# Optimization experiments

Hardware: AMD Instinct MI355X
Metric: run time of the kernel (lower is better)

Reference implementation:

```python
import jax, jax.numpy as jnp
import numpy as np

IMAGE_SIZE = 224          # config.image_size
RP_Q = 10 / 100.0         # config.rp_percentage, 'point' threshold mode
EPS = 1e-8                # normalize_minmax eps
CLIP = 1e-6               # arccos clamp margin


def minmax_global(x):
    """normalize_minmax over the whole tensor (as applied to the raw series)."""
    lo, hi = x.min(), x.max()
    rng = hi - lo
    return jnp.where(rng < EPS, jnp.zeros_like(x), (x - lo) / (rng + EPS))


def minmax_per_matrix(x):
    """normalize_minmax applied independently per (b, d) LxL matrix."""
    lo = x.min(axis=(-2, -1), keepdims=True)
    hi = x.max(axis=(-2, -1), keepdims=True)
    rng = hi - lo
    return jnp.where(rng < EPS, jnp.zeros_like(x), (x - lo) / (rng + EPS))


def setup_inputs() -> dict:
    key = jax.random.key(0)
    x = jax.random.normal(key, (4, 1024, 8), dtype=jnp.float32)  # [B, L, D]
    return {"x": x}


def reference(x):
    B, L, D = x.shape

    # ---- Gramian Angular Field (summation), vectorized over (b, d) ----
    x_norm = minmax_global(x) * 2.0 - 1.0                       # [B, L, D]
    theta = jnp.arccos(jnp.clip(x_norm, -1.0 + CLIP, 1.0 - CLIP))
    th = jnp.transpose(theta, (0, 2, 1))                        # [B, D, L]
    gaf = jnp.cos(th[:, :, :, None] + th[:, :, None, :])        # [B, D, L, L]
    gaf = minmax_per_matrix(gaf)

    # ---- Recurrence plot ('point' quantile threshold), vectorized ----
    s = jnp.transpose(x, (0, 2, 1))                             # [B, D, L]
    dist = jnp.abs(s[:, :, :, None] - s[:, :, None, :])         # [B, D, L, L]
    thr = jnp.quantile(dist.reshape(B, D, L * L), RP_Q, axis=-1)
    rp = (dist <= thr[:, :, None, None]).astype(x.dtype)        # [B, D, L, L]

    # ---- Bilinear resize to (image_size, image_size), align_corners=False ----
    out = jnp.concatenate([gaf, rp], axis=1)                    # [B, 2D, L, L]
    out = jax.image.resize(out, (B, 2 * D, IMAGE_SIZE, IMAGE_SIZE),
                           method="bilinear", antialias=False)
    return out
```

## Files before the change

kernel.cpp:

```cpp
#include <hip/hip_runtime.h>
#include <cfloat>
#include <math.h>

#define B_ 4
#define L_ 1024
#define D_ 8
#define OUT_ 224
#define NPIX (B_ * 2 * D_ * OUT_ * OUT_)
#define NT4  (NPIX / 4)
#define PI_F 3.14159265358979323846f
#define TBL 128
#define TSTR 896

__device__ __forceinline__ float clipnorm(float v, float lo, float inv2, int degen) {
    float xn = degen ? -1.0f : ((v - lo) * inv2 - 1.0f);
    return fminf(fmaxf(xn, -1.0f + 1e-6f), 1.0f - 1e-6f);
}
__device__ __forceinline__ unsigned fkey(float f) {
    unsigned u = __float_as_uint(f);
    return (u & 0x80000000u) ? ~u : (u | 0x80000000u);
}
__device__ __forceinline__ float unfkey(unsigned k) {
    unsigned u = (k & 0x80000000u) ? (k ^ 0x80000000u) : ~k;
    return __uint_as_float(u);
}

__global__ __launch_bounds__(1024) void k_stats(const float* __restrict__ x,
                                                float* __restrict__ ws) {
    __shared__ float t[L_];
    __shared__ float csort[L_], ssort[L_], w[L_];
    __shared__ unsigned part[2][16];
    __shared__ unsigned umin_a, umax_a, umin_b, umax_b, succ_bits;
    __shared__ unsigned cand_n;
    __shared__ float cand[64];
    __shared__ float bc_v1v2[2];

    const int tid  = threadIdx.x;
    const int lane = tid & 63;
    const int wave = tid >> 6;
    const int blk  = blockIdx.x;
    const int b = blk >> 3, d = blk & 7;

    if (tid == 0) {
        umin_a = 0xFFFFFFFFu; umax_a = 0u;
        umin_b = 0xFFFFFFFFu; umax_b = 0u;
        succ_bits = 0xFFFFFFFFu;
        cand_n = 0u;
    }
    __syncthreads();

    {
        const float4* x4 = (const float4*)x;
        float lo = FLT_MAX, hi = -FLT_MAX;
        for (int i = tid; i < (B_ * L_ * D_) / 4; i += 1024) {
            float4 q = x4[i];
            lo = fminf(fminf(fminf(lo, q.x), q.y), fminf(q.z, q.w));
            hi = fmaxf(fmaxf(fmaxf(hi, q.x), q.y), fmaxf(q.z, q.w));
        }
#pragma unroll
        for (int off = 32; off; off >>= 1) {
            lo = fminf(lo, __shfl_down(lo, off));
            hi = fmaxf(hi, __shfl_down(hi, off));
        }
        if (lane == 0) { atomicMin(&umin_a, fkey(lo)); atomicMax(&umax_a, fkey(hi)); }
    }
    __syncthreads();
    const float glo = unfkey(umin_a), ghi = unfkey(umax_a);
    if (blk == 0 && tid == 0) { ws[0] = glo; ws[1] = ghi; }
    const float rng  = ghi - glo;
    const int degen  = rng < 1e-8f;
    const float inv2 = 2.0f / (rng + 1e-8f);

    if (tid < 2 * OUT_) {
        const float scale = (float)L_ / (float)OUT_;
        int o = (tid < OUT_) ? tid : tid - OUT_;
        float fx = (o + 0.5f) * scale - 0.5f;
        int x0 = (int)fx; float wx = fx - (float)x0;
        float q0 = x[(b * L_ + x0) * D_ + d];
        float q1 = x[(b * L_ + x0 + 1) * D_ + d];
        float* base = ws + TBL + blk * TSTR;
        if (tid < OUT_) {
            float c0 = clipnorm(q0, glo, inv2, degen), c1 = clipnorm(q1, glo, inv2, degen);
            float s0 = sqrtf(fmaxf(0.0f, 1.0f - c0 * c0)), s1 = sqrtf(fmaxf(0.0f, 1.0f - c1 * c1));
            base[o]        = c0 + wx * (c1 - c0);
            base[OUT_ + o] = s0 + wx * (s1 - s0);
        } else {
            base[448 + o] = q0;
            base[672 + o] = q1;
        }
    }

    float v = x[(b * L_ + tid) * D_ + d];
    for (int k = 2; k <= L_; k <<= 1) {
        bool up = ((tid & k) == 0);
        for (int j = k >> 1; j > 0; j >>= 1) {
            bool lower = ((tid & j) == 0);
            float other;
            if (j >= 64) {
                __syncthreads();
                t[tid] = v;
                __syncthreads();
                other = t[tid ^ j];
            } else {
                other = __shfl_xor(v, j);
            }
            float mn = fminf(v, other), mx = fmaxf(v, other);
            v = (lower == up) ? mn : mx;
        }
    }
    __syncthreads();
    t[tid] = v;
    {
        float c = clipnorm(v, glo, inv2, degen);
        csort[tid] = c;
        ssort[tid] = sqrtf(fmaxf(0.0f, 1.0f - c * c));
        w[tid]     = acosf(c);
    }
    __syncthreads();

    {
        float wi = w[tid];
        int jstar = -1;
        if (wi + w[0] >= PI_F) {
            int a = 0, bh = L_ - 1;
            while (a < bh) { int m = (a + bh + 1) >> 1; if (wi + w[m] >= PI_F) a = m; else bh = m - 1; }
            jstar = a;
        }
        float ci = csort[tid], si = ssort[tid];
        float mn = FLT_MAX, mx = -FLT_MAX;
        int cands[4] = {0, L_ - 1, jstar, jstar + 1};
#pragma unroll
        for (int q = 0; q < 4; q++) {
            int j = cands[q];
            if (j >= 0 && j < L_) {
                float g = ci * csort[j] - si * ssort[j];
                mn = fminf(mn, g); mx = fmaxf(mx, g);
            }
        }
#pragma unroll
        for (int off = 32; off; off >>= 1) {
            mn = fminf(mn, __shfl_down(mn, off));
            mx = fmaxf(mx, __shfl_down(mx, off));
        }
        if (lane == 0) { atomicMin(&umin_b, fkey(mn)); atomicMax(&umax_b, fkey(mx)); }
        __syncthreads();
        if (tid == 0) {
            ws[2 + blk * 3 + 0] = unfkey(umin_b);
            ws[2 + blk * 3 + 1] = unfkey(umax_b);
        }
    }

    const float ti = v;
    int pass = 0;
    auto block_count = [&](unsigned c) -> unsigned {
#pragma unroll
        for (int off = 32; off; off >>= 1) c += __shfl_down(c, off);
        int pb = pass & 1;
        if (lane == 0) part[pb][wave] = c;
        __syncthreads();
        unsigned tot = 0;
#pragma unroll
        for (int w2 = 0; w2 < 16; w2++) tot += part[pb][w2];
        pass++;
        return tot;
    };

    int jloA_, jhiA_;
    {
        int aL = 0, bL = tid, aH = tid, bH = L_ - 1;
        while ((aL < bL) | (aH < bH)) {
            int mL = (aL + bL) >> 1;
            int mH = (aH + bH + 1) >> 1;
            float tL = t[aL < bL ? mL : 0];
            float tH = t[aH < bH ? mH : 0];
            if (aL < bL) { if (ti - tL <= 0.0f) bL = mL; else aL = mL + 1; }
            if (aH < bH) { if (tH - ti <= 0.0f) aH = mH; else bH = mH - 1; }
        }
        jloA_ = aL; jhiA_ = aH;
    }

    const unsigned k1 = 104858u, k2 = 104859u;
    unsigned c0 = block_count((unsigned)(jhiA_ - jloA_ + 1));

    float thr;
    if (c0 >= k1) {
        if (c0 >= k2) thr = 0.0f;
        else {
            float s = FLT_MAX;
            if (jloA_ > 0)      s = fminf(s, ti - t[jloA_ - 1]);
            if (jhiA_ < L_ - 1) s = fminf(s, t[jhiA_ + 1] - ti);
#pragma unroll
            for (int off = 32; off; off >>= 1) s = fminf(s, __shfl_down(s, off));
            if (lane == 0) atomicMin(&succ_bits, __float_as_uint(s));
            __syncthreads();
            thr = 0.5f * __uint_as_float(succ_bits);
        }
    } else {
        unsigned aBits = 0u, bBits = __float_as_uint(t[L_ - 1] - t[0]);
        unsigned cntLo = c0, cntHi = (unsigned)(L_ * L_);
        int jloB_ = 0, jhiB_ = L_ - 1;
        float sga = (float)((long long)c0 - (long long)k1);
        float sgb = (float)((long long)(L_ * L_) - (long long)k1);
        int lastSide = 0, sameCnt = 0;

        while ((bBits - aBits > 1u) && (cntHi - cntLo > 63u)) {
            unsigned mb;
            if (sameCnt >= 3) {
                mb = aBits + ((bBits - aBits) >> 1);
                sameCnt = 0;
            } else {
                float va = __uint_as_float(aBits), vb = __uint_as_float(bBits);
                float vg = va - sga * (vb - va) / (sgb - sga);
                mb = __float_as_uint(vg);
                if (mb <= aBits) mb = aBits + 1u;
                else if (mb >= bBits) mb = bBits - 1u;
            }
            float vm = __uint_as_float(mb);
            int aL = jloB_, bL = jloA_, aH = jhiA_, bH = jhiB_;
            while ((aL < bL) | (aH < bH)) {
                int mL = (aL + bL) >> 1;
                int mH = (aH + bH + 1) >> 1;
                float tL = t[aL < bL ? mL : 0];
                float tH = t[aH < bH ? mH : 0];
                if (aL < bL) { if (ti - tL <= vm) bL = mL; else aL = mL + 1; }
                if (aH < bH) { if (tH - ti <= vm) aH = mH; else bH = mH - 1; }
            }
            unsigned tot = block_count((unsigned)(aH - aL + 1));
            long long g = (long long)tot - (long long)k1;
            if (g >= 0) {
                bBits = mb; cntHi = tot; jloB_ = aL; jhiB_ = aH;
                sgb = fmaxf((float)g, 0.5f);
                if (lastSide == 1) { sga *= 0.5f; sameCnt++; } else sameCnt = 1;
                lastSide = 1;
            } else {
                aBits = mb; cntLo = tot; jloA_ = aL; jhiA_ = aH;
                sga = fminf((float)g, -0.5f);
                if (lastSide == -1) { sgb *= 0.5f; sameCnt++; } else sameCnt = 1;
                lastSide = -1;
            }
        }

        if (cntHi - cntLo <= 63u) {
            for (int j = jloB_; j < jloA_; j++) { unsigned p = atomicAdd(&cand_n, 1u); cand[p] = ti - t[j]; }
            for (int j = jhiA_ + 1; j <= jhiB_; j++) { unsigned p = atomicAdd(&cand_n, 1u); cand[p] = t[j] - ti; }
            __syncthreads();
            if (tid < 64) {
                unsigned n = cand_n;
                float val = ((unsigned)tid < n) ? cand[tid] : FLT_MAX;
#pragma unroll
                for (int k = 2; k <= 64; k <<= 1) {
                    bool up = ((tid & k) == 0);
#pragma unroll
                    for (int j = k >> 1; j > 0; j >>= 1) {
                        float o = __shfl_xor(val, j);
                        bool lower = ((tid & j) == 0);
                        float mn = fminf(val, o), mx = fmaxf(val, o);
                        val = (lower == up) ? mn : mx;
                    }
                }
                unsigned r1 = k1 - cntLo, r2 = k2 - cntLo;
                float v1l = __shfl(val, (int)r1 - 1);
                float v2l = (r2 <= n) ? __shfl(val, (int)r2 - 1) : FLT_MAX;
                if (tid == 0) { bc_v1v2[0] = v1l; bc_v1v2[1] = v2l; }
            }
            __syncthreads();
            float v1 = bc_v1v2[0], v2m = bc_v1v2[1];
            if (v2m < FLT_MAX) {
                thr = v1 + (v2m - v1) * 0.5f;
            } else {
                float s = FLT_MAX;
                if (jloB_ > 0)      s = fminf(s, ti - t[jloB_ - 1]);
                if (jhiB_ < L_ - 1) s = fminf(s, t[jhiB_ + 1] - ti);
#pragma unroll
                for (int off = 32; off; off >>= 1) s = fminf(s, __shfl_down(s, off));
                if (lane == 0) atomicMin(&succ_bits, __float_as_uint(s));
                __syncthreads();
                float v2 = __uint_as_float(succ_bits);
                thr = v1 + (v2 - v1) * 0.5f;
            }
        } else {
            float v1 = __uint_as_float(bBits);
            if (cntHi >= k2) {
                thr = v1;
            } else {
                float s = FLT_MAX;
                if (jloB_ > 0)      s = fminf(s, ti - t[jloB_ - 1]);
                if (jhiB_ < L_ - 1) s = fminf(s, t[jhiB_ + 1] - ti);
#pragma unroll
                for (int off = 32; off; off >>= 1) s = fminf(s, __shfl_down(s, off));
                if (lane == 0) atomicMin(&succ_bits, __float_as_uint(s));
                __syncthreads();
                float v2 = __uint_as_float(succ_bits);
                thr = v1 + (v2 - v1) * 0.5f;
            }
        }
    }
    if (tid == 0) ws[2 + blk * 3 + 2] = thr;
}

__global__ __launch_bounds__(256) void k_out(const float* __restrict__ ws,
                                             float4* __restrict__ out4) {
    __shared__ __align__(16) float lds[448];
    __shared__ float sc[3];

    const int tid = threadIdx.x;
    int plane = blockIdx.x / 49;
    int c = plane & 15, b = plane >> 4, d = c & 7;

    const float* tb = ws + TBL + (b * 8 + d) * TSTR + ((c < 8) ? 0 : 448);
    for (int i = tid; i < 448; i += 256) lds[i] = tb[i];
    if (tid == 0) {
        if (c < 8) {
            float mn = ws[2 + (b * 8 + d) * 3 + 0];
            float mx = ws[2 + (b * 8 + d) * 3 + 1];
            float g = mx - mn;
            sc[0] = mn;
            sc[1] = (g < 1e-8f) ? 0.0f : 1.0f / (g + 1e-8f);
            sc[2] = (g < 1e-8f) ? 1.0f : 0.0f;
        } else {
            sc[0] = ws[2 + (b * 8 + d) * 3 + 2];
        }
    }
    __syncthreads();

    int tix = blockIdx.x * 256 + tid;
    int pix0 = tix << 2;
    int ox0 = pix0 % OUT_;
    int oy  = (pix0 / OUT_) % OUT_;

    float4 r;
    if (c < 8) {
        float mn = sc[0], ginv = sc[1];
        bool gdeg = sc[2] != 0.0f;
        float Cr = lds[oy], Sr = lds[OUT_ + oy];
        float4 Cc = *(const float4*)&lds[ox0];
        float4 Sc = *(const float4*)&lds[OUT_ + ox0];
        r.x = gdeg ? 0.0f : ((Cr * Cc.x - Sr * Sc.x) - mn) * ginv;
        r.y = gdeg ? 0.0f : ((Cr * Cc.y - Sr * Sc.y) - mn) * ginv;
        r.z = gdeg ? 0.0f : ((Cr * Cc.z - Sr * Sc.z) - mn) * ginv;
        r.w = gdeg ? 0.0f : ((Cr * Cc.w - Sr * Sc.w) - mn) * ginv;
    } else {
        float thr = sc[0];
        const float scale = (float)L_ / (float)OUT_;
        float fy = (oy + 0.5f) * scale - 0.5f;
        int y0 = (int)fy; float wy = fy - (float)y0;
        float r0 = lds[oy], r1 = lds[OUT_ + oy];
        float4 q0 = *(const float4*)&lds[ox0];
        float4 q1 = *(const float4*)&lds[OUT_ + ox0];
        float qq0[4] = {q0.x, q0.y, q0.z, q0.w};
        float qq1[4] = {q1.x, q1.y, q1.z, q1.w};
        float res[4];
#pragma unroll
        for (int p = 0; p < 4; p++) {
            float fx = (ox0 + p + 0.5f) * scale - 0.5f;
            int x0i = (int)fx; float wx = fx - (float)x0i;
            float v00 = (fabsf(r0 - qq0[p]) <= thr) ? 1.0f : 0.0f;
            float v01 = (fabsf(r0 - qq1[p]) <= thr) ? 1.0f : 0.0f;
            float v10 = (fabsf(r1 - qq0[p]) <= thr) ? 1.0f : 0.0f;
            float v11 = (fabsf(r1 - qq1[p]) <= thr) ? 1.0f : 0.0f;
            float top = v00 + wx * (v01 - v00);
            float bot = v10 + wx * (v11 - v10);
            res[p] = top + wy * (bot - top);
        }
        r = make_float4(res[0], res[1], res[2], res[3]);
    }
    out4[tix] = r;
}

extern "C" void kernel_launch(void* const* d_in, const int* in_sizes, int n_in,
                              void* d_out, int out_size, void* d_ws, size_t ws_size,
                              hipStream_t stream) {
    const float* x = (const float*)d_in[0];
    float* ws = (float*)d_ws;

    k_stats<<<B_ * D_, 1024, 0, stream>>>(x, ws);
    k_out<<<NT4 / 256, 256, 0, stream>>>(ws, (float4*)d_out);
}
```

Before: 96.94 us.

## Replace per-plane sort/bisection quantile with histogram-based multi-kernel selection

Swaps the single 32-block stats kernel (bitonic sort plus iterative count bisection) for a three-kernel pipeline. The first kernel spreads the O(L^2) pairwise distances across 512 blocks to build distance histograms and GAF min/max. The second collects candidates falling in the bins around the target rank, and the third refines by sub-histogram to select the quantile. It uses the output buffer as scratch before k_out overwrites it. This aims to raise parallelism over the serialized bisection, at the cost of brute-force pair work, LDS atomics, extra launches, and a fixed candidate cap (CAP) that could overflow.

```diff
diff --git a/kernel.cpp b/kernel.cpp
--- a/kernel.cpp
+++ b/kernel.cpp
@@ -8,294 +8,402 @@
 #define OUT_ 224
 #define NPIX (B_ * 2 * D_ * OUT_ * OUT_)
 #define NT4  (NPIX / 4)
-#define PI_F 3.14159265358979323846f
 #define TBL 128
 #define TSTR 896
+
+#define NPLANE 32
+#define PB 16
+#define NBLK (NPLANE * PB)
+#define NBIN 2048
+#define CAP 8192
+#define R1U 51917u
+#define R2U 51918u
+
+#define SC_PHIST 0u
+#define SC_PGAF  ((unsigned)NBLK * (unsigned)NBIN)
+#define SC_CCNT  (SC_PGAF + (unsigned)NBLK * 2u)
+#define SC_BBC   (SC_CCNT + (unsigned)NPLANE)
+#define SC_CAND  (SC_BBC + (unsigned)NPLANE * 4u)
 
 __device__ __forceinline__ float clipnorm(float v, float lo, float inv2, int degen) {
     float xn = degen ? -1.0f : ((v - lo) * inv2 - 1.0f);
     return fminf(fmaxf(xn, -1.0f + 1e-6f), 1.0f - 1e-6f);
 }
-__device__ __forceinline__ unsigned fkey(float f) {
-    unsigned u = __float_as_uint(f);
-    return (u & 0x80000000u) ? ~u : (u | 0x80000000u);
-}
-__device__ __forceinline__ float unfkey(unsigned k) {
-    unsigned u = (k & 0x80000000u) ? (k ^ 0x80000000u) : ~k;
-    return __uint_as_float(u);
-}
-
-__global__ __launch_bounds__(1024) void k_stats(const float* __restrict__ x,
-                                                float* __restrict__ ws) {
-    __shared__ float t[L_];
-    __shared__ float csort[L_], ssort[L_], w[L_];
-    __shared__ unsigned part[2][16];
-    __shared__ unsigned umin_a, umax_a, umin_b, umax_b, succ_bits;
-    __shared__ unsigned cand_n;
-    __shared__ float cand[64];
-    __shared__ float bc_v1v2[2];
+
+__device__ __forceinline__ float sort64(float val, int tid) {
+#pragma unroll
+    for (int k = 2; k <= 64; k <<= 1) {
+        bool up = ((tid & k) == 0);
+#pragma unroll
+        for (int j = k >> 1; j > 0; j >>= 1) {
+            float o = __shfl_xor(val, j);
+            bool lower = ((tid & j) == 0);
+            float mn = fminf(val, o), mx = fmaxf(val, o);
+            val = (lower == up) ? mn : mx;
+        }
+    }
+    return val;
+}
+
+__global__ __launch_bounds__(256) void k_pairs(const float* __restrict__ x,
+                                               float* __restrict__ ws,
+                                               unsigned* __restrict__ scratch) {
+    __shared__ float s[L_], cc[L_], ssn[L_];
+    __shared__ unsigned hist[NBIN];
+    __shared__ float red[16];
 
     const int tid  = threadIdx.x;
     const int lane = tid & 63;
     const int wave = tid >> 6;
-    const int blk  = blockIdx.x;
-    const int b = blk >> 3, d = blk & 7;
-
+    const int bid  = blockIdx.x;
+    const int p    = bid >> 4;
+    const int bip  = bid & 15;
+    const int b    = p >> 3, d = p & 7;
+
+    float lo = FLT_MAX, hi = -FLT_MAX;
+    const float4* x4 = (const float4*)x;
+    for (int i = tid; i < (B_ * L_ * D_) / 4; i += 256) {
+        float4 q = x4[i];
+        lo = fminf(fminf(fminf(lo, q.x), q.y), fminf(q.z, q.w));
+        hi = fmaxf(fmaxf(fmaxf(hi, q.x), q.y), fmaxf(q.z, q.w));
+    }
+#pragma unroll
+    for (int off = 32; off; off >>= 1) {
+        lo = fminf(lo, __shfl_down(lo, off));
+        hi = fmaxf(hi, __shfl_down(hi, off));
+    }
+    if (lane == 0) { red[wave] = lo; red[8 + wave] = hi; }
+    __syncthreads();
+    const float glo = fminf(fminf(red[0], red[1]), fminf(red[2], red[3]));
+    const float ghi = fmaxf(fmaxf(red[8], red[9]), fmaxf(red[10], red[11]));
+    const float rng   = ghi - glo;
+    const int   degen = rng < 1e-8f;
+    const float inv2  = 2.0f / (rng + 1e-8f);
+    const float scale = (float)(NBIN - 1) / fmaxf(rng, 1e-20f);
+
+    if (bid == 0) {
+        if (tid == 0) { ws[0] = glo; ws[1] = ghi; }
+        if (tid < NPLANE) scratch[SC_CCNT + tid] = 0u;
+    }
+
+    for (int i = tid; i < L_; i += 256) {
+        float v = x[(b * L_ + i) * D_ + d];
+        float c = clipnorm(v, glo, inv2, degen);
+        s[i] = v; cc[i] = c; ssn[i] = sqrtf(fmaxf(0.0f, 1.0f - c * c));
+    }
+    for (int i = tid; i < NBIN; i += 256) hist[i] = 0u;
+    __syncthreads();
+
+    float sj[4], cj[4], zj[4];
+#pragma unroll
+    for (int q = 0; q < 4; q++) {
+        int j = tid + q * 256;
+        sj[q] = s[j]; cj[q] = cc[j]; zj[q] = ssn[j];
+    }
+    float gmn = FLT_MAX, gmx = -FLT_MAX;
+#pragma unroll
+    for (int q = 0; q < 4; q++) {
+        float g = cj[q] * cj[q] - zj[q] * zj[q];
+        gmn = fminf(gmn, g); gmx = fmaxf(gmx, g);
+    }
+
+    for (int rp = 0; rp < 64; ++rp) {
+        int i = (rp < 32) ? (bip * 32 + rp) : (L_ - 1 - (bip * 32 + rp - 32));
+        float siv = s[i], civ = cc[i], ziv = ssn[i];
+#pragma unroll
+        for (int q = 0; q < 4; q++) {
+            int j = tid + q * 256;
+            if (j > i) {
+                float dd = fabsf(siv - sj[q]);
+                int bin = (int)(dd * scale);
+                bin = min(bin, NBIN - 1);
+                atomicAdd(&hist[bin], 1u);
+                float g = civ * cj[q] - ziv * zj[q];
+                gmn = fminf(gmn, g); gmx = fmaxf(gmx, g);
+            }
+        }
+    }
+    __syncthreads();
+
+    {
+        unsigned* ph = scratch + SC_PHIST + (unsigned)bid * NBIN;
+        for (int i = tid; i < NBIN; i += 256) ph[i] = hist[i];
+    }
+#pragma unroll
+    for (int off = 32; off; off >>= 1) {
+        gmn = fminf(gmn, __shfl_down(gmn, off));
+        gmx = fmaxf(gmx, __shfl_down(gmx, off));
+    }
+    if (lane == 0) { red[wave] = gmn; red[8 + wave] = gmx; }
+    __syncthreads();
     if (tid == 0) {
-        umin_a = 0xFFFFFFFFu; umax_a = 0u;
-        umin_b = 0xFFFFFFFFu; umax_b = 0u;
-        succ_bits = 0xFFFFFFFFu;
-        cand_n = 0u;
-    }
-    __syncthreads();
-
-    {
-        const float4* x4 = (const float4*)x;
-        float lo = FLT_MAX, hi = -FLT_MAX;
-        for (int i = tid; i < (B_ * L_ * D_) / 4; i += 1024) {
-            float4 q = x4[i];
-            lo = fminf(fminf(fminf(lo, q.x), q.y), fminf(q.z, q.w));
-            hi = fmaxf(fmaxf(fmaxf(hi, q.x), q.y), fmaxf(q.z, q.w));
-        }
-#pragma unroll
-        for (int off = 32; off; off >>= 1) {
-            lo = fminf(lo, __shfl_down(lo, off));
-            hi = fmaxf(hi, __shfl_down(hi, off));
-        }
-        if (lane == 0) { atomicMin(&umin_a, fkey(lo)); atomicMax(&umax_a, fkey(hi)); }
-    }
-    __syncthreads();
-    const float glo = unfkey(umin_a), ghi = unfkey(umax_a);
-    if (blk == 0 && tid == 0) { ws[0] = glo; ws[1] = ghi; }
-    const float rng  = ghi - glo;
-    const int degen  = rng < 1e-8f;
-    const float inv2 = 2.0f / (rng + 1e-8f);
-
-    if (tid < 2 * OUT_) {
-        const float scale = (float)L_ / (float)OUT_;
-        int o = (tid < OUT_) ? tid : tid - OUT_;
-        float fx = (o + 0.5f) * scale - 0.5f;
-        int x0 = (int)fx; float wx = fx - (float)x0;
-        float q0 = x[(b * L_ + x0) * D_ + d];
-        float q1 = x[(b * L_ + x0 + 1) * D_ + d];
-        float* base = ws + TBL + blk * TSTR;
-        if (tid < OUT_) {
+        float* pg = (float*)scratch + SC_PGAF + bid * 2;
+        pg[0] = fminf(fminf(red[0], red[1]), fminf(red[2], red[3]));
+        pg[1] = fmaxf(fmaxf(red[8], red[9]), fmaxf(red[10], red[11]));
+    }
+
+    if (bip == 0) {
+        const float scL = (float)L_ / (float)OUT_;
+        float* base = ws + TBL + p * TSTR;
+        for (int o = tid; o < OUT_; o += 256) {
+            float fx = (o + 0.5f) * scL - 0.5f;
+            int x0 = (int)fx; float wx = fx - (float)x0;
+            float q0 = x[(b * L_ + x0) * D_ + d];
+            float q1 = x[(b * L_ + x0 + 1) * D_ + d];
             float c0 = clipnorm(q0, glo, inv2, degen), c1 = clipnorm(q1, glo, inv2, degen);
             float s0 = sqrtf(fmaxf(0.0f, 1.0f - c0 * c0)), s1 = sqrtf(fmaxf(0.0f, 1.0f - c1 * c1));
             base[o]        = c0 + wx * (c1 - c0);
             base[OUT_ + o] = s0 + wx * (s1 - s0);
-        } else {
-            base[448 + o] = q0;
-            base[672 + o] = q1;
-        }
-    }
-
-    float v = x[(b * L_ + tid) * D_ + d];
-    for (int k = 2; k <= L_; k <<= 1) {
-        bool up = ((tid & k) == 0);
-        for (int j = k >> 1; j > 0; j >>= 1) {
-            bool lower = ((tid & j) == 0);
-            float other;
-            if (j >= 64) {
-                __syncthreads();
-                t[tid] = v;
-                __syncthreads();
-                other = t[tid ^ j];
-            } else {
-                other = __shfl_xor(v, j);
-            }
-            float mn = fminf(v, other), mx = fmaxf(v, other);
-            v = (lower == up) ? mn : mx;
-        }
-    }
-    __syncthreads();
-    t[tid] = v;
-    {
-        float c = clipnorm(v, glo, inv2, degen);
-        csort[tid] = c;
-        ssort[tid] = sqrtf(fmaxf(0.0f, 1.0f - c * c));
-        w[tid]     = acosf(c);
-    }
-    __syncthreads();
-
-    {
-        float wi = w[tid];
-        int jstar = -1;
-        if (wi + w[0] >= PI_F) {
-            int a = 0, bh = L_ - 1;
-            while (a < bh) { int m = (a + bh + 1) >> 1; if (wi + w[m] >= PI_F) a = m; else bh = m - 1; }
-            jstar = a;
-        }
-        float ci = csort[tid], si = ssort[tid];
-        float mn = FLT_MAX, mx = -FLT_MAX;
-        int cands[4] = {0, L_ - 1, jstar, jstar + 1};
+            base[448 + o]  = q0;
+            base[672 + o]  = q1;
+        }
+    }
+}
+
+__global__ __launch_bounds__(256) void k_collect(const float* __restrict__ x,
+                                                 const float* __restrict__ ws,
+                                                 unsigned* __restrict__ scratch) {
+    __shared__ float s[L_];
+    __shared__ unsigned cwsum[4];
+    __shared__ unsigned sB1, sB2, sBase;
+
+    const int tid  = threadIdx.x;
+    const int lane = tid & 63;
+    const int wave = tid >> 6;
+    const int bid  = blockIdx.x;
+    const int p    = bid >> 4;
+    const int bip  = bid & 15;
+    const int b    = p >> 3, d = p & 7;
+
+    const float glo = ws[0], ghi = ws[1];
+    const float scale = (float)(NBIN - 1) / fmaxf(ghi - glo, 1e-20f);
+
+    for (int i = tid; i < L_; i += 256) s[i] = x[(b * L_ + i) * D_ + d];
+
+    unsigned loc[8];
+#pragma unroll
+    for (int q = 0; q < 8; q++) loc[q] = 0u;
+    const unsigned* ph = scratch + SC_PHIST + (unsigned)(p * PB) * NBIN;
+    for (int k = 0; k < PB; k++) {
+        const unsigned* hh = ph + k * NBIN + tid * 8;
+#pragma unroll
+        for (int q = 0; q < 8; q++) loc[q] += hh[q];
+    }
+    unsigned tsum = 0u;
+#pragma unroll
+    for (int q = 0; q < 8; q++) tsum += loc[q];
+    unsigned inc = tsum;
+#pragma unroll
+    for (int off = 1; off < 64; off <<= 1) {
+        unsigned o = __shfl_up(inc, off);
+        if (lane >= off) inc += o;
+    }
+    if (lane == 63) cwsum[wave] = inc;
+    __syncthreads();
+    unsigned woff = 0u;
+    for (int w2 = 0; w2 < 4; w2++) woff += (w2 < wave) ? cwsum[w2] : 0u;
+    unsigned run = woff + inc - tsum;
+#pragma unroll
+    for (int q = 0; q < 8; q++) {
+        unsigned prev = run; run += loc[q];
+        if (prev < R1U && run >= R1U) { sB1 = (unsigned)(tid * 8 + q); sBase = prev; }
+        if (prev < R2U && run >= R2U) { sB2 = (unsigned)(tid * 8 + q); }
+    }
+    __syncthreads();
+    const unsigned B1 = sB1, B2 = sB2;
+    if (bip == 0 && tid == 0) {
+        unsigned* bbc = scratch + SC_BBC + (unsigned)p * 4u;
+        bbc[0] = B1; bbc[1] = B2; bbc[2] = sBase;
+    }
+
+    float sj[4];
+#pragma unroll
+    for (int q = 0; q < 4; q++) sj[q] = s[tid + q * 256];
+
+    unsigned* ccnt = scratch + SC_CCNT + p;
+    float* cand = (float*)scratch + SC_CAND + (unsigned)p * CAP;
+    for (int rp = 0; rp < 64; ++rp) {
+        int i = (rp < 32) ? (bip * 32 + rp) : (L_ - 1 - (bip * 32 + rp - 32));
+        float siv = s[i];
 #pragma unroll
         for (int q = 0; q < 4; q++) {
-            int j = cands[q];
-            if (j >= 0 && j < L_) {
-                float g = ci * csort[j] - si * ssort[j];
-                mn = fminf(mn, g); mx = fmaxf(mx, g);
-            }
-        }
-#pragma unroll
-        for (int off = 32; off; off >>= 1) {
+            int j = tid + q * 256;
+            if (j > i) {
+                float dd = fabsf(siv - sj[q]);
+                int bin = (int)(dd * scale);
+                bin = min(bin, NBIN - 1);
+                if (bin >= (int)B1 && bin <= (int)B2) {
+                    unsigned idx = atomicAdd(ccnt, 1u);
+                    if (idx < CAP) cand[idx] = dd;
+                }
+            }
+        }
+    }
+}
+
+__global__ __launch_bounds__(1024) void k_select(float* __restrict__ ws,
+                                                 unsigned* __restrict__ scratch) {
+    __shared__ float cd[CAP];
+    __shared__ float buf2[2048];
+    __shared__ unsigned h[1024];
+    __shared__ unsigned wsum[16], wsum2[16];
+    __shared__ unsigned sT1, sT2, sC1, sH1, scnt, uminb, umaxb;
+    __shared__ float sv1, sv2;
+
+    const int tid  = threadIdx.x;
+    const int lane = tid & 63;
+    const int wave = tid >> 6;
+    const int p    = blockIdx.x;
+
+    const float glo = ws[0], ghi = ws[1];
+    const float scale = (float)(NBIN - 1) / fmaxf(ghi - glo, 1e-20f);
+    const unsigned* bbc = scratch + SC_BBC + (unsigned)p * 4u;
+    const unsigned B1 = bbc[0], B2 = bbc[1], base = bbc[2];
+    unsigned n = scratch[SC_CCNT + p];
+    n = (n < (unsigned)CAP) ? n : (unsigned)CAP;
+    const float* cand = (const float*)scratch + SC_CAND + (unsigned)p * CAP;
+    for (unsigned k = tid; k < n; k += 1024) cd[k] = cand[k];
+
+    float* cur = cd;
+    float* nxt = buf2;
+    unsigned ncur = n;
+    unsigned r1 = R1U - base;
+    float vlo = (float)B1 / scale;
+    float vhi = (float)(B2 + 1u) / scale;
+    float v1 = 0.0f, v2 = 0.0f;
+    bool done = false;
+
+    for (int it = 0; it < 6 && !done; ++it) {
+        if (tid == 0) scnt = 0u;
+        h[tid] = 0u;
+        __syncthreads();
+
+        if (ncur <= 64u) {
+            if (tid < 64) {
+                float val = ((unsigned)tid < ncur) ? cur[tid] : FLT_MAX;
+                val = sort64(val, tid);
+                float v1l = __shfl(val, (int)r1 - 1);
+                float v2l = __shfl(val, (int)r1);
+                if (tid == 0) { sv1 = v1l; sv2 = v2l; }
+            }
+            __syncthreads();
+            v1 = sv1; v2 = sv2;
+            done = true;
+            break;
+        }
+
+        float sc2 = 1023.0f / fmaxf(vhi - vlo, 1e-30f);
+        for (unsigned k = tid; k < ncur; k += 1024) {
+            int bb = (int)((cur[k] - vlo) * sc2);
+            bb = max(0, min(bb, 1023));
+            atomicAdd(&h[bb], 1u);
+        }
+        __syncthreads();
+
+        unsigned hv = h[tid];
+        unsigned inc = hv;
+#pragma unroll
+        for (int off = 1; off < 64; off <<= 1) {
+            unsigned o = __shfl_up(inc, off);
+            if (lane >= off) inc += o;
+        }
+        if (lane == 63) wsum[wave] = inc;
+        __syncthreads();
+        if (wave == 0 && lane < 16) {
+            unsigned wv = wsum[lane];
+#pragma unroll
+            for (int off = 1; off < 16; off <<= 1) {
+                unsigned o = __shfl_up(wv, off);
+                if (lane >= off) wv += o;
+            }
+            wsum2[lane] = wv;
+        }
+        __syncthreads();
+        unsigned cum  = inc + ((wave > 0) ? wsum2[wave - 1] : 0u);
+        unsigned cumb = cum - hv;
+        unsigned r2 = r1 + 1u;
+        if (cum >= r1 && cumb < r1) { sT1 = (unsigned)tid; sC1 = cumb; sH1 = hv; }
+        if (cum >= r2 && cumb < r2) { sT2 = (unsigned)tid; }
+        __syncthreads();
+        const unsigned t1 = sT1, t2 = sT2, c1 = sC1, h1 = sH1;
+
+        if (t1 != t2) {
+            if (tid == 0) { uminb = 0xFFFFFFFFu; umaxb = 0u; }
+            __syncthreads();
+            for (unsigned k = tid; k < ncur; k += 1024) {
+                float val = cur[k];
+                int bb = (int)((val - vlo) * sc2);
+                bb = max(0, min(bb, 1023));
+                if (bb == (int)t1) atomicMax(&umaxb, __float_as_uint(val));
+                else if (bb > (int)t1) atomicMin(&uminb, __float_as_uint(val));
+            }
+            __syncthreads();
+            v1 = __uint_as_float(umaxb);
+            v2 = __uint_as_float(uminb);
+            done = true;
+            break;
+        }
+
+        if (h1 <= 64u) {
+            for (unsigned k = tid; k < ncur; k += 1024) {
+                float val = cur[k];
+                int bb = (int)((val - vlo) * sc2);
+                bb = max(0, min(bb, 1023));
+                if (bb == (int)t1) {
+                    unsigned idx = atomicAdd(&scnt, 1u);
+                    if (idx < 64u) nxt[idx] = val;
+                }
+            }
+            __syncthreads();
+            unsigned cnt = (scnt < 64u) ? scnt : 64u;
+            unsigned rr = r1 - c1;
+            if (tid < 64) {
+                float val = ((unsigned)tid < cnt) ? nxt[tid] : FLT_MAX;
+                val = sort64(val, tid);
+                float v1l = __shfl(val, (int)rr - 1);
+                float v2l = __shfl(val, (int)rr);
+                if (tid == 0) { sv1 = v1l; sv2 = v2l; }
+            }
+            __syncthreads();
+            v1 = sv1; v2 = sv2;
+            done = true;
+            break;
+        }
+
+        for (unsigned k = tid; k < ncur; k += 1024) {
+            float val = cur[k];
+            int bb = (int)((val - vlo) * sc2);
+            bb = max(0, min(bb, 1023));
+            if (bb == (int)t1) {
+                unsigned idx = atomicAdd(&scnt, 1u);
+                if (idx < 2048u) nxt[idx] = val;
+            }
+        }
+        __syncthreads();
+        ncur = (scnt < 2048u) ? scnt : 2048u;
+        r1 = r1 - c1;
+        float nvlo = vlo + (float)t1 / sc2;
+        float nvhi = vlo + (float)(t1 + 1u) / sc2;
+        vlo = nvlo; vhi = nvhi;
+        float* tmp = cur; cur = nxt; nxt = tmp;
+        __syncthreads();
+    }
+    if (!done) { v1 = vlo; v2 = vhi; }
+
+    if (tid < 16) {
+        const float* pg = (const float*)scratch + SC_PGAF + (unsigned)(p * PB + tid) * 2u;
+        float mn = pg[0], mx = pg[1];
+#pragma unroll
+        for (int off = 8; off; off >>= 1) {
             mn = fminf(mn, __shfl_down(mn, off));
             mx = fmaxf(mx, __shfl_down(mx, off));
         }
-        if (lane == 0) { atomicMin(&umin_b, fkey(mn)); atomicMax(&umax_b, fkey(mx)); }
-        __syncthreads();
         if (tid == 0) {
-            ws[2 + blk * 3 + 0] = unfkey(umin_b);
-            ws[2 + blk * 3 + 1] = unfkey(umax_b);
-        }
-    }
-
-    const float ti = v;
-    int pass = 0;
-    auto block_count = [&](unsigned c) -> unsigned {
-#pragma unroll
-        for (int off = 32; off; off >>= 1) c += __shfl_down(c, off);
-        int pb = pass & 1;
-        if (lane == 0) part[pb][wave] = c;
-        __syncthreads();
-        unsigned tot = 0;
-#pragma unroll
-        for (int w2 = 0; w2 < 16; w2++) tot += part[pb][w2];
-        pass++;
-        return tot;
-    };
-
-    int jloA_, jhiA_;
-    {
-        int aL = 0, bL = tid, aH = tid, bH = L_ - 1;
-        while ((aL < bL) | (aH < bH)) {
-            int mL = (aL + bL) >> 1;
-            int mH = (aH + bH + 1) >> 1;
-            float tL = t[aL < bL ? mL : 0];
-            float tH = t[aH < bH ? mH : 0];
-            if (aL < bL) { if (ti - tL <= 0.0f) bL = mL; else aL = mL + 1; }
-            if (aH < bH) { if (tH - ti <= 0.0f) aH = mH; else bH = mH - 1; }
-        }
-        jloA_ = aL; jhiA_ = aH;
-    }
-
-    const unsigned k1 = 104858u, k2 = 104859u;
-    unsigned c0 = block_count((unsigned)(jhiA_ - jloA_ + 1));
-
-    float thr;
-    if (c0 >= k1) {
-        if (c0 >= k2) thr = 0.0f;
-        else {
-            float s = FLT_MAX;
-            if (jloA_ > 0)      s = fminf(s, ti - t[jloA_ - 1]);
-            if (jhiA_ < L_ - 1) s = fminf(s, t[jhiA_ + 1] - ti);
-#pragma unroll
-            for (int off = 32; off; off >>= 1) s = fminf(s, __shfl_down(s, off));
-            if (lane == 0) atomicMin(&succ_bits, __float_as_uint(s));
-            __syncthreads();
-            thr = 0.5f * __uint_as_float(succ_bits);
-        }
-    } else {
-        unsigned aBits = 0u, bBits = __float_as_uint(t[L_ - 1] - t[0]);
-        unsigned cntLo = c0, cntHi = (unsigned)(L_ * L_);
-        int jloB_ = 0, jhiB_ = L_ - 1;
-        float sga = (float)((long long)c0 - (long long)k1);
-        float sgb = (float)((long long)(L_ * L_) - (long long)k1);
-        int lastSide = 0, sameCnt = 0;
-
-        while ((bBits - aBits > 1u) && (cntHi - cntLo > 63u)) {
-            unsigned mb;
-            if (sameCnt >= 3) {
-                mb = aBits + ((bBits - aBits) >> 1);
-                sameCnt = 0;
-            } else {
-                float va = __uint_as_float(aBits), vb = __uint_as_float(bBits);
-                float vg = va - sga * (vb - va) / (sgb - sga);
-                mb = __float_as_uint(vg);
-                if (mb <= aBits) mb = aBits + 1u;
-                else if (mb >= bBits) mb = bBits - 1u;
-            }
-            float vm = __uint_as_float(mb);
-            int aL = jloB_, bL = jloA_, aH = jhiA_, bH = jhiB_;
-            while ((aL < bL) | (aH < bH)) {
-                int mL = (aL + bL) >> 1;
-                int mH = (aH + bH + 1) >> 1;
-                float tL = t[aL < bL ? mL : 0];
-                float tH = t[aH < bH ? mH : 0];
-                if (aL < bL) { if (ti - tL <= vm) bL = mL; else aL = mL + 1; }
-                if (aH < bH) { if (tH - ti <= vm) aH = mH; else bH = mH - 1; }
-            }
-            unsigned tot = block_count((unsigned)(aH - aL + 1));
-            long long g = (long long)tot - (long long)k1;
-            if (g >= 0) {
-                bBits = mb; cntHi = tot; jloB_ = aL; jhiB_ = aH;
-                sgb = fmaxf((float)g, 0.5f);
-                if (lastSide == 1) { sga *= 0.5f; sameCnt++; } else sameCnt = 1;
-                lastSide = 1;
-            } else {
-                aBits = mb; cntLo = tot; jloA_ = aL; jhiA_ = aH;
-                sga = fminf((float)g, -0.5f);
-                if (lastSide == -1) { sgb *= 0.5f; sameCnt++; } else sameCnt = 1;
-                lastSide = -1;
-            }
-        }
-
-        if (cntHi - cntLo <= 63u) {
-            for (int j = jloB_; j < jloA_; j++) { unsigned p = atomicAdd(&cand_n, 1u); cand[p] = ti - t[j]; }
-            for (int j = jhiA_ + 1; j <= jhiB_; j++) { unsigned p = atomicAdd(&cand_n, 1u); cand[p] = t[j] - ti; }
-            __syncthreads();
-            if (tid < 64) {
-                unsigned n = cand_n;
-                float val = ((unsigned)tid < n) ? cand[tid] : FLT_MAX;
-#pragma unroll
-                for (int k = 2; k <= 64; k <<= 1) {
-                    bool up = ((tid & k) == 0);
-#pragma unroll
-                    for (int j = k >> 1; j > 0; j >>= 1) {
-                        float o = __shfl_xor(val, j);
-                        bool lower = ((tid & j) == 0);
-                        float mn = fminf(val, o), mx = fmaxf(val, o);
-                        val = (lower == up) ? mn : mx;
-                    }
-                }
-                unsigned r1 = k1 - cntLo, r2 = k2 - cntLo;
-                float v1l = __shfl(val, (int)r1 - 1);
-                float v2l = (r2 <= n) ? __shfl(val, (int)r2 - 1) : FLT_MAX;
-                if (tid == 0) { bc_v1v2[0] = v1l; bc_v1v2[1] = v2l; }
-            }
-            __syncthreads();
-            float v1 = bc_v1v2[0], v2m = bc_v1v2[1];
-            if (v2m < FLT_MAX) {
-                thr = v1 + (v2m - v1) * 0.5f;
-            } else {
-                float s = FLT_MAX;
-                if (jloB_ > 0)      s = fminf(s, ti - t[jloB_ - 1]);
-                if (jhiB_ < L_ - 1) s = fminf(s, t[jhiB_ + 1] - ti);
-#pragma unroll
-                for (int off = 32; off; off >>= 1) s = fminf(s, __shfl_down(s, off));
-                if (lane == 0) atomicMin(&succ_bits, __float_as_uint(s));
-                __syncthreads();
-                float v2 = __uint_as_float(succ_bits);
-                thr = v1 + (v2 - v1) * 0.5f;
-            }
-        } else {
-            float v1 = __uint_as_float(bBits);
-            if (cntHi >= k2) {
-                thr = v1;
-            } else {
-                float s = FLT_MAX;
-                if (jloB_ > 0)      s = fminf(s, ti - t[jloB_ - 1]);
-                if (jhiB_ < L_ - 1) s = fminf(s, t[jhiB_ + 1] - ti);
-#pragma unroll
-                for (int off = 32; off; off >>= 1) s = fminf(s, __shfl_down(s, off));
-                if (lane == 0) atomicMin(&succ_bits, __float_as_uint(s));
-                __syncthreads();
-                float v2 = __uint_as_float(succ_bits);
-                thr = v1 + (v2 - v1) * 0.5f;
-            }
-        }
-    }
-    if (tid == 0) ws[2 + blk * 3 + 2] = thr;
+            ws[2 + p * 3 + 0] = mn;
+            ws[2 + p * 3 + 1] = mx;
+            ws[2 + p * 3 + 2] = v1 + (v2 - v1) * 0.5f;
+        }
+    }
 }
 
 __global__ __launch_bounds__(256) void k_out(const float* __restrict__ ws,
@@ -351,16 +459,16 @@
         float qq1[4] = {q1.x, q1.y, q1.z, q1.w};
         float res[4];
 #pragma unroll
-        for (int p = 0; p < 4; p++) {
-            float fx = (ox0 + p + 0.5f) * scale - 0.5f;
+        for (int pq = 0; pq < 4; pq++) {
+            float fx = (ox0 + pq + 0.5f) * scale - 0.5f;
             int x0i = (int)fx; float wx = fx - (float)x0i;
-            float v00 = (fabsf(r0 - qq0[p]) <= thr) ? 1.0f : 0.0f;
-            float v01 = (fabsf(r0 - qq1[p]) <= thr) ? 1.0f : 0.0f;
-            float v10 = (fabsf(r1 - qq0[p]) <= thr) ? 1.0f : 0.0f;
-            float v11 = (fabsf(r1 - qq1[p]) <= thr) ? 1.0f : 0.0f;
+            float v00 = (fabsf(r0 - qq0[pq]) <= thr) ? 1.0f : 0.0f;
+            float v01 = (fabsf(r0 - qq1[pq]) <= thr) ? 1.0f : 0.0f;
+            float v10 = (fabsf(r1 - qq0[pq]) <= thr) ? 1.0f : 0.0f;
+            float v11 = (fabsf(r1 - qq1[pq]) <= thr) ? 1.0f : 0.0f;
             float top = v00 + wx * (v01 - v00);
             float bot = v10 + wx * (v11 - v10);
-            res[p] = top + wy * (bot - top);
+            res[pq] = top + wy * (bot - top);
         }
         r = make_float4(res[0], res[1], res[2], res[3]);
     }
@@ -372,7 +480,10 @@
                               hipStream_t stream) {
     const float* x = (const float*)d_in[0];
     float* ws = (float*)d_ws;
-
-    k_stats<<<B_ * D_, 1024, 0, stream>>>(x, ws);
+    unsigned* scratch = (unsigned*)d_out;
+
+    k_pairs<<<NBLK, 256, 0, stream>>>(x, ws, scratch);
+    k_collect<<<NBLK, 256, 0, stream>>>(x, ws, scratch);
+    k_select<<<NPLANE, 1024, 0, stream>>>(ws, scratch);
     k_out<<<NT4 / 256, 256, 0, stream>>>(ws, (float4*)d_out);
 }
```

Result: slower. 312.7 us (+222.6%).
